# Optimization experiments

Hardware: AMD Instinct MI355X
Metric: run time of the kernel (lower is better)

The kernel has to match this reference:

```python
import jax, jax.numpy as jnp
import numpy as np

N, E = 50000, 800000
IN, HID, OUT, HEADS = 256, 128, 256, 4
CAT = HEADS * HID  # 512


def _gat(x, ei_src, ei_dst, W, a_src, a_dst, b, heads, out_ch, concat):
    """PyG-style GATConv with self-loops. x:[N,F]; returns [N,heads*out_ch] or [N,out_ch]."""
    n = x.shape[0]
    loop = jnp.arange(n, dtype=ei_src.dtype)
    src = jnp.concatenate([ei_src, loop])
    dst = jnp.concatenate([ei_dst, loop])
    h = (x @ W).reshape(n, heads, out_ch)              # [N,H,C]
    al_s = jnp.einsum('nhc,hc->nh', h, a_src)          # [N,H]
    al_d = jnp.einsum('nhc,hc->nh', h, a_dst)
    e = jax.nn.leaky_relu(al_s[src] + al_d[dst], 0.2)  # [E',H]
    emax = jax.ops.segment_max(e, dst, num_segments=n)
    ee = jnp.exp(e - emax[dst])
    denom = jax.ops.segment_sum(ee, dst, num_segments=n)
    alpha = ee / (denom[dst] + 1e-16)                  # segment softmax over incoming edges
    out = jax.ops.segment_sum(h[src] * alpha[:, :, None], dst, num_segments=n)  # [N,H,C]
    out = out.reshape(n, heads * out_ch) if concat else out.mean(axis=1)
    return out + b


def setup_inputs() -> dict:
    key = jax.random.key(0)
    ks = jax.random.split(key, 20)
    g = lambda k, shape, fan: (jax.random.normal(k, shape, jnp.float32) / np.sqrt(fan)).astype(jnp.float32)
    return {
        'x': jax.random.normal(ks[0], (N, IN), jnp.float32),
        'edge_index': jax.random.randint(ks[1], (2, E), 0, N, dtype=jnp.int32),
        # GAT layer 1: IN -> HID x 4 heads, concat
        'W1': g(ks[2], (IN, CAT), IN), 'a_src1': g(ks[3], (HEADS, HID), HID),
        'a_dst1': g(ks[4], (HEADS, HID), HID), 'b1': jnp.zeros((CAT,), jnp.float32),
        # GAT layer 2: CAT -> HID x 4 heads, concat
        'W2': g(ks[5], (CAT, CAT), CAT), 'a_src2': g(ks[6], (HEADS, HID), HID),
        'a_dst2': g(ks[7], (HEADS, HID), HID), 'b2': jnp.zeros((CAT,), jnp.float32),
        # GAT layer 3: CAT -> OUT, 1 head, no concat
        'W3': g(ks[8], (CAT, OUT), CAT), 'a_src3': g(ks[9], (1, OUT), OUT),
        'a_dst3': g(ks[10], (1, OUT), OUT), 'b3': jnp.zeros((OUT,), jnp.float32),
        # response_generator MLP: OUT -> 2*HID -> HID -> OUT
        'M1': g(ks[11], (OUT, 2 * HID), OUT), 'mb1': jnp.zeros((2 * HID,), jnp.float32),
        'M2': g(ks[12], (2 * HID, HID), 2 * HID), 'mb2': jnp.zeros((HID,), jnp.float32),
        'M3': g(ks[13], (HID, OUT), HID), 'mb3': jnp.zeros((OUT,), jnp.float32),
    }


def reference(x, edge_index, W1, a_src1, a_dst1, b1, W2, a_src2, a_dst2, b2,
              W3, a_src3, a_dst3, b3, M1, mb1, M2, mb2, M3, mb3):
    src, dst = edge_index[0], edge_index[1]
    h = _gat(x, src, dst, W1, a_src1, a_dst1, b1, HEADS, HID, True)
    h = jax.nn.elu(h)  # dropout is identity in eval mode
    h = _gat(h, src, dst, W2, a_src2, a_dst2, b2, HEADS, HID, True)
    h = jax.nn.elu(h)
    h = _gat(h, src, dst, W3, a_src3, a_dst3, b3, 1, OUT, False)
    # response generator MLP (dropout identity in eval)
    r = jax.nn.relu(h @ M1 + mb1)
    r = jax.nn.relu(r @ M2 + mb2)
    return r @ M3 + mb3
```

## Files before the change

### kernel.cpp

```cpp
#include <hip/hip_runtime.h>
#include <cstdint>
#include <cstddef>

#define HEADS  4
#define HIDC   128
#define CATF   512
#define IN_F   256
#define OUT_F  256

typedef _Float16 f16x8 __attribute__((ext_vector_type(8)));
typedef _Float16 f16x4 __attribute__((ext_vector_type(4)));
typedef float f32x4  __attribute__((ext_vector_type(4)));

__device__ __forceinline__ void async16(const void* g, void* l) {
    __builtin_amdgcn_global_load_lds((const __attribute__((address_space(1))) void*)g,
                                     (__attribute__((address_space(3))) void*)l, 16, 0, 0);
}

__global__ void init_counts(int* cnt, int N) {
    int i = blockIdx.x * blockDim.x + threadIdx.x;
    if (i < N) cnt[i] = 1;
}

__global__ void count_dst(const int* __restrict__ dst, int E, int* cnt) {
    int i = blockIdx.x * blockDim.x + threadIdx.x;
    if (i < E) atomicAdd(&cnt[dst[i]], 1);
}

__global__ void scan_partial(const int* __restrict__ cnt, int* excl, int* bsum, int N) {
    __shared__ int tmp[256];
    int i = blockIdx.x * 256 + threadIdx.x;
    int v = (i < N) ? cnt[i] : 0;
    tmp[threadIdx.x] = v;
    __syncthreads();
    for (int off = 1; off < 256; off <<= 1) {
        int t = ((int)threadIdx.x >= off) ? tmp[threadIdx.x - off] : 0;
        __syncthreads();
        tmp[threadIdx.x] += t;
        __syncthreads();
    }
    if (i < N) excl[i] = tmp[threadIdx.x] - v;
    if (threadIdx.x == 255) bsum[blockIdx.x] = tmp[255];
}

__global__ void scan_bsums(int* bsum, int nb) {
    __shared__ int tmp[256];
    int v = ((int)threadIdx.x < nb) ? bsum[threadIdx.x] : 0;
    tmp[threadIdx.x] = v;
    __syncthreads();
    for (int off = 1; off < 256; off <<= 1) {
        int t = ((int)threadIdx.x >= off) ? tmp[threadIdx.x - off] : 0;
        __syncthreads();
        tmp[threadIdx.x] += t;
        __syncthreads();
    }
    if ((int)threadIdx.x < nb) bsum[threadIdx.x] = tmp[threadIdx.x] - v;
}

__global__ void add_carry(int* indptr, int* pos, const int* __restrict__ bsum, int N, int total) {
    int i = blockIdx.x * blockDim.x + threadIdx.x;
    if (i < N) {
        int v = indptr[i] + bsum[i >> 8];
        indptr[i] = v;
        pos[i] = v;
    }
    if (i == 0) indptr[N] = total;
}

__global__ void scatter_edges(const int* __restrict__ src, const int* __restrict__ dst,
                              int E, int N, int* pos, int* esrc) {
    int i = blockIdx.x * blockDim.x + threadIdx.x;
    int total = E + N;
    if (i >= total) return;
    int s, d;
    if (i < E) { s = src[i]; d = dst[i]; }
    else       { s = i - E;  d = s; }
    int p = atomicAdd(&pos[d], 1);
    esrc[p] = s;
}

__global__ void conv_h16(const float* __restrict__ in, _Float16* __restrict__ out, long n4) {
    long i = (long)blockIdx.x * blockDim.x + threadIdx.x;
    if (i >= n4) return;
    float4 v = ((const float4*)in)[i];
    f16x4 o = { (_Float16)v.x, (_Float16)v.y, (_Float16)v.z, (_Float16)v.w };
    ((f16x4*)out)[i] = o;
}

struct WDesc { const float* W; _Float16* hi; _Float16* lo; int K; int N; int off; };
struct WPack { WDesc d[6]; int total; };
__global__ void conv_w_all(WPack p) {
    int idx = blockIdx.x * blockDim.x + threadIdx.x;
    if (idx >= p.total) return;
    int wi = 0;
    while (wi < 5 && idx >= p.d[wi + 1].off) wi++;
    const WDesc& w = p.d[wi];
    int li = idx - w.off;
    int n = li / w.K, k = li - n * w.K;
    float v = w.W[(size_t)k * w.N + n];
    _Float16 h = (_Float16)v;
    w.hi[(size_t)n * w.K + k] = h;
    if (w.lo) w.lo[(size_t)n * w.K + k] = (_Float16)(v - (float)h);
}

__global__ void zero2(float* a, float* b, int n) {
    int i = blockIdx.x * blockDim.x + threadIdx.x;
    if (i < n) { a[i] = 0.f; b[i] = 0.f; }
}

#define TM 128
#define TN 128
#define TK 32
template <int MODE, int NMF, int ATTN>
__global__ __launch_bounds__(256) void gemm_bt(
        const _Float16* __restrict__ A,
        const _Float16* __restrict__ Bh, const _Float16* __restrict__ Bl,
        const float* __restrict__ bias,
        float* __restrict__ out_f, _Float16* __restrict__ out_h16,
        const float* __restrict__ asrc, const float* __restrict__ adst,
        float* __restrict__ al_s, float* __restrict__ al_d,
        int M, int N, int K, int act) {
    __shared__ __align__(16) char smem[(NMF == 2 ? 49152 : 32768) + (ATTN ? 2048 : 16)];
    _Float16* sA  = (_Float16*)smem;
    _Float16* sBh = (_Float16*)(smem + 16384);
    _Float16* sBl = (_Float16*)(smem + 32768);
    float* sred   = (float*)(smem + (NMF == 2 ? 49152 : 32768));

    int tid = threadIdx.x;
    int wave = tid >> 6, lane = tid & 63;
    int nwg = gridDim.x * gridDim.y;
    int id  = blockIdx.y * gridDim.x + blockIdx.x;
    int qq = nwg >> 3, rr = nwg & 7;
    int xcd = id & 7, li = id >> 3;
    int wg = (xcd < rr ? xcd * (qq + 1) : rr * (qq + 1) + (xcd - rr) * qq) + li;
    int by = wg / (int)gridDim.x;
    int bx = wg - by * (int)gridDim.x;
    int m0 = by * TM, n0 = bx * TN;
    int wm = wave >> 1, wn = wave & 1;
    int srow = lane >> 2;
    int skel = (lane & 3) * 8;
    int fr = lane & 15, quad = lane >> 4;

    f32x4 acc[4][4];
#pragma unroll
    for (int i = 0; i < 4; i++)
#pragma unroll
        for (int j = 0; j < 4; j++) acc[i][j] = (f32x4){0.f, 0.f, 0.f, 0.f};

    auto stage = [&](int buf, int k0) {
#pragma unroll
        for (int c = 0; c < 2; c++) {
            int chunk = wave * 2 + c;
            int r = chunk * 16 + srow;
            int gmA = m0 + r; if (gmA >= M) gmA = M - 1;
            int gnB = n0 + r;
            size_t aoff = (size_t)gmA * K + k0 + skel;
            size_t boff = (size_t)gnB * K + k0 + skel;
            int ldso = buf * (TM * TK) + chunk * 512;
            async16(A + aoff, &sA[ldso]);
            async16(Bh + boff, &sBh[ldso]);
            if (NMF == 2) async16(Bl + boff, &sBl[ldso]);
        }
    };

    const int nsteps = K / TK;
    stage(0, 0);
    int cur = 0;
    for (int s = 0; s < nsteps; ++s, cur ^= 1) {
        if (s + 1 < nsteps) {
            stage(cur ^ 1, (s + 1) * TK);
            if (NMF == 2) asm volatile("s_waitcnt vmcnt(6)" ::: "memory");
            else          asm volatile("s_waitcnt vmcnt(4)" ::: "memory");
        } else {
            asm volatile("s_waitcnt vmcnt(0)" ::: "memory");
        }
        __builtin_amdgcn_s_barrier();
        __builtin_amdgcn_sched_barrier(0);

        f16x8 fa[4], fbh[4], fbl[4];
#pragma unroll
        for (int i = 0; i < 4; i++) {
            int ra = cur * (TM * TK) + (wm * 64 + i * 16 + fr) * TK + quad * 8;
            int rb = cur * (TN * TK) + (wn * 64 + i * 16 + fr) * TK + quad * 8;
            fa[i]  = *(const f16x8*)&sA[ra];
            fbh[i] = *(const f16x8*)&sBh[rb];
            if (NMF == 2) fbl[i] = *(const f16x8*)&sBl[rb];
        }
#pragma unroll
        for (int i = 0; i < 4; i++)
#pragma unroll
            for (int j = 0; j < 4; j++) {
                if (NMF == 2)
                    acc[i][j] = __builtin_amdgcn_mfma_f32_16x16x32_f16(fa[i], fbl[j], acc[i][j], 0, 0, 0);
                acc[i][j] = __builtin_amdgcn_mfma_f32_16x16x32_f16(fa[i], fbh[j], acc[i][j], 0, 0, 0);
            }
        __builtin_amdgcn_sched_barrier(0);
        __builtin_amdgcn_s_barrier();
    }

    float avs[4], avd[4], bv[4];
#pragma unroll
    for (int j = 0; j < 4; j++) {
        int gn = n0 + wn * 64 + j * 16 + fr;
        if (ATTN) { avs[j] = asrc[gn]; avd[j] = adst[gn]; }
        bv[j] = bias ? bias[gn] : 0.f;
    }

    if (ATTN) {
#pragma unroll
        for (int i = 0; i < 4; i++)
#pragma unroll
            for (int r = 0; r < 4; r++) {
                float ps = 0.f, pd = 0.f;
#pragma unroll
                for (int j = 0; j < 4; j++) {
                    float v = acc[i][j][r];
                    ps += v * avs[j]; pd += v * avd[j];
                }
#pragma unroll
                for (int off = 1; off < 16; off <<= 1) {
                    ps += __shfl_xor(ps, off);
                    pd += __shfl_xor(pd, off);
                }
                if (fr == 0) {
                    int lrow = wm * 64 + i * 16 + quad * 4 + r;
                    sred[lrow * 4 + 0 * 2 + wn] = ps;
                    sred[lrow * 4 + 1 * 2 + wn] = pd;
                }
            }
    }

    if (MODE == 1) {
#pragma unroll
        for (int i = 0; i < 4; i++)
#pragma unroll
            for (int r = 0; r < 4; r++) {
                int gm = m0 + wm * 64 + i * 16 + quad * 4 + r;
                if (gm >= M) continue;
#pragma unroll
                for (int j = 0; j < 4; j++) {
                    int gn = n0 + wn * 64 + j * 16 + fr;
                    float v = acc[i][j][r] + bv[j];
                    if (act == 1) v = fmaxf(v, 0.f);
                    out_f[(size_t)gm * N + gn] = v;
                }
            }
        __syncthreads();
    } else {
        _Float16* cst = (_Float16*)smem;
#pragma unroll
        for (int i = 0; i < 4; i++) {
            int svb = ((wm * 16 + i * 4 + quad) << 1) & 15;
#pragma unroll
            for (int j = 0; j < 4; j++) {
#pragma unroll
                for (int r = 0; r < 4; r++) {
                    int row = wm * 64 + i * 16 + quad * 4 + r;
                    int col = wn * 64 + j * 16 + fr;
                    float v = acc[i][j][r] + bv[j];
                    if (act == 1) v = fmaxf(v, 0.f);
                    int blk = (col >> 3) ^ svb;
                    cst[row * 128 + (blk << 3) + (col & 7)] = (_Float16)v;
                }
            }
        }
        __syncthreads();
#pragma unroll
        for (int q = 0; q < 8; q++) {
            int c = tid + 256 * q;
            int row = c >> 4, b = c & 15;
            int gm = m0 + row;
            if (gm < M) {
                int svb = ((row >> 2) << 1) & 15;
                f16x8 val = *(const f16x8*)&cst[row * 128 + ((b ^ svb) << 3)];
                *(f16x8*)&out_h16[(size_t)gm * N + n0 + b * 8] = val;
            }
        }
    }

    if (ATTN) {
        if (tid < TM) {
            int gm = m0 + tid;
            if (gm < M) {
                float s = sred[tid * 4 + 0] + sred[tid * 4 + 1];
                float d = sred[tid * 4 + 2] + sred[tid * 4 + 3];
                if (ATTN == 1) {
                    int head = n0 >> 7;
                    al_s[gm * HEADS + head] = s;
                    al_d[gm * HEADS + head] = d;
                } else {
                    atomicAdd(&al_s[gm], s);
                    atomicAdd(&al_d[gm], d);
                }
            }
        }
    }
}

template <int CT, int H>
__global__ void gat_aggregate_f(const _Float16* __restrict__ h,
                                const float* __restrict__ al_s, const float* __restrict__ al_d,
                                const int* __restrict__ indptr, const int* __restrict__ esrc,
                                const float* __restrict__ bias,
                                _Float16* __restrict__ oh,
                                int N, int act) {
    typedef _Float16 hvec __attribute__((ext_vector_type(CT)));
    const int C_ALL = CT * 64;
    int n = (blockIdx.x * blockDim.x + threadIdx.x) >> 6;
    int lane = threadIdx.x & 63;
    if (n >= N) return;
    int head = (lane * H) >> 6;
    float ald = al_d[n * H + head];
    float acc[CT];
#pragma unroll
    for (int k = 0; k < CT; k++) acc[k] = 0.f;
    float dsum = 0.f;

    int beg = indptr[n], end = indptr[n + 1];
    int idx = beg;
    for (; idx + 8 <= end; idx += 8) {
        int s[8]; float av[8]; hvec v[8];
#pragma unroll
        for (int u = 0; u < 8; u++) s[u] = esrc[idx + u];
#pragma unroll
        for (int u = 0; u < 8; u++) av[u] = al_s[s[u] * H + head];
#pragma unroll
        for (int u = 0; u < 8; u++) v[u] = *(const hvec*)(h + (size_t)s[u] * C_ALL + lane * CT);
#pragma unroll
        for (int u = 0; u < 8; u++) {
            float e = av[u] + ald;
            e = e > 0.f ? e : 0.2f * e;
            e = fminf(e, 60.f);
            float w = __expf(e);
            dsum += w;
#pragma unroll
            for (int k = 0; k < CT; k++) acc[k] += w * (float)v[u][k];
        }
    }
    if (idx + 4 <= end) {
        int s[4]; float av[4]; hvec v[4];
#pragma unroll
        for (int u = 0; u < 4; u++) s[u] = esrc[idx + u];
#pragma unroll
        for (int u = 0; u < 4; u++) av[u] = al_s[s[u] * H + head];
#pragma unroll
        for (int u = 0; u < 4; u++) v[u] = *(const hvec*)(h + (size_t)s[u] * C_ALL + lane * CT);
#pragma unroll
        for (int u = 0; u < 4; u++) {
            float e = av[u] + ald;
            e = e > 0.f ? e : 0.2f * e;
            e = fminf(e, 60.f);
            float w = __expf(e);
            dsum += w;
#pragma unroll
            for (int k = 0; k < CT; k++) acc[k] += w * (float)v[u][k];
        }
        idx += 4;
    }
    for (; idx < end; idx++) {
        int s0 = esrc[idx];
        float e = al_s[s0 * H + head] + ald;
        e = e > 0.f ? e : 0.2f * e;
        e = fminf(e, 60.f);
        float w = __expf(e);
        dsum += w;
        hvec v0 = *(const hvec*)(h + (size_t)s0 * C_ALL + lane * CT);
#pragma unroll
        for (int k = 0; k < CT; k++) acc[k] += w * (float)v0[k];
    }

    float inv = 1.f / (dsum + 1e-16f);
    size_t ob = (size_t)n * C_ALL + lane * CT;
    const float* bp = bias + lane * CT;
    hvec o;
#pragma unroll
    for (int k = 0; k < CT; k++) {
        float v = acc[k] * inv + bp[k];
        if (act == 1) v = v > 0.f ? v : (__expf(v) - 1.f);
        o[k] = (_Float16)v;
    }
    __builtin_nontemporal_store(o, (hvec*)(oh + ob));
}

extern "C" void kernel_launch(void* const* d_in, const int* in_sizes, int n_in,
                              void* d_out, int out_size, void* d_ws, size_t ws_size,
                              hipStream_t stream) {
    const float* x   = (const float*)d_in[0];
    const int*   ei  = (const int*)d_in[1];
    const float* W1  = (const float*)d_in[2];
    const float* as1 = (const float*)d_in[3];
    const float* ad1 = (const float*)d_in[4];
    const float* b1  = (const float*)d_in[5];
    const float* W2  = (const float*)d_in[6];
    const float* as2 = (const float*)d_in[7];
    const float* ad2 = (const float*)d_in[8];
    const float* b2  = (const float*)d_in[9];
    const float* W3  = (const float*)d_in[10];
    const float* as3 = (const float*)d_in[11];
    const float* ad3 = (const float*)d_in[12];
    const float* b3  = (const float*)d_in[13];
    const float* M1  = (const float*)d_in[14];
    const float* mb1 = (const float*)d_in[15];
    const float* M2  = (const float*)d_in[16];
    const float* mb2 = (const float*)d_in[17];
    const float* M3  = (const float*)d_in[18];
    const float* mb3 = (const float*)d_in[19];
    float* out = (float*)d_out;

    const int N = in_sizes[0] / IN_F;
    const int E = in_sizes[1] / 2;
    const int* src = ei;
    const int* dst = ei + E;

    char* ws = (char*)d_ws;
    auto alloc = [&](size_t bytes) { char* p = ws; ws += (bytes + 255) & ~(size_t)255; return p; };
    _Float16* H16 = (_Float16*)alloc((size_t)N * CATF * 2);
    _Float16* P16 = (_Float16*)alloc((size_t)N * CATF * 2);
    float* al_s = (float*)alloc((size_t)N * HEADS * 4);
    float* al_d = (float*)alloc((size_t)N * HEADS * 4);
    int* cnt    = (int*)alloc((size_t)N * 4);
    int* pos    = (int*)alloc((size_t)N * 4);
    int* indptr = (int*)alloc((size_t)(N + 1) * 4);
    int* esrc   = (int*)alloc((size_t)(E + N) * 4);
    int* bsum   = (int*)alloc(256 * 4);
    auto walloc = [&](int k, int n, _Float16*& h, _Float16*& l, bool need_lo) {
        h = (_Float16*)alloc((size_t)k * n * 2);
        l = need_lo ? (_Float16*)alloc((size_t)k * n * 2) : nullptr;
    };
    _Float16 *W1h, *W1l, *W2h, *W2l, *W3h, *W3l, *M1h, *M1l, *M2h, *M2l, *M3h, *M3l;
    walloc(IN_F, CATF, W1h, W1l, false);
    walloc(CATF, CATF, W2h, W2l, false);
    walloc(CATF, OUT_F, W3h, W3l, false);
    walloc(OUT_F, 2 * HIDC, M1h, M1l, true);
    walloc(2 * HIDC, HIDC, M2h, M2l, true);
    walloc(HIDC, OUT_F, M3h, M3l, true);

    const int nb = (N + 255) / 256;
    init_counts<<<(N + 255) / 256, 256, 0, stream>>>(cnt, N);
    count_dst<<<(E + 255) / 256, 256, 0, stream>>>(dst, E, cnt);
    scan_partial<<<nb, 256, 0, stream>>>(cnt, indptr, bsum, N);
    scan_bsums<<<1, 256, 0, stream>>>(bsum, nb);
    add_carry<<<nb, 256, 0, stream>>>(indptr, pos, bsum, N, E + N);
    scatter_edges<<<(E + N + 255) / 256, 256, 0, stream>>>(src, dst, E, N, pos, esrc);

    {
        WPack p;
        int off = 0;
        auto setd = [&](int i, const float* W, _Float16* h, _Float16* l, int K, int Nc) {
            p.d[i] = WDesc{W, h, l, K, Nc, off};
            off += K * Nc;
        };
        setd(0, W1, W1h, W1l, IN_F, CATF);
        setd(1, W2, W2h, W2l, CATF, CATF);
        setd(2, W3, W3h, W3l, CATF, OUT_F);
        setd(3, M1, M1h, M1l, OUT_F, 2 * HIDC);
        setd(4, M2, M2h, M2l, 2 * HIDC, HIDC);
        setd(5, M3, M3h, M3l, HIDC, OUT_F);
        p.total = off;
        conv_w_all<<<(off + 255) / 256, 256, 0, stream>>>(p);
    }

    auto gemm_gat = [&](const _Float16* Ap, const _Float16* Bhp, _Float16* oh,
                        const float* asrc, const float* adst, int M_, int Nc, int K, int attn_mode) {
        dim3 grid(Nc / TN, (M_ + TM - 1) / TM);
        if (attn_mode == 1)
            gemm_bt<2, 1, 1><<<grid, 256, 0, stream>>>(Ap, Bhp, nullptr, nullptr, nullptr, oh,
                                                       asrc, adst, al_s, al_d, M_, Nc, K, 0);
        else
            gemm_bt<2, 1, 2><<<grid, 256, 0, stream>>>(Ap, Bhp, nullptr, nullptr, nullptr, oh,
                                                       asrc, adst, al_s, al_d, M_, Nc, K, 0);
    };
    auto gemm_mlp16 = [&](const _Float16* Ap, const _Float16* Bhp, const _Float16* Blp,
                          const float* bias, _Float16* oh, int M_, int Nc, int K, int act) {
        dim3 grid(Nc / TN, (M_ + TM - 1) / TM);
        gemm_bt<2, 2, 0><<<grid, 256, 0, stream>>>(Ap, Bhp, Blp, bias, nullptr, oh,
                                                   nullptr, nullptr, nullptr, nullptr, M_, Nc, K, act);
    };

    const int gwav = (N + 3) / 4;

    conv_h16<<<((long)N * IN_F / 4 + 255) / 256, 256, 0, stream>>>(x, P16, (long)N * IN_F / 4);

    gemm_gat(P16, W1h, H16, as1, ad1, N, CATF, IN_F, 1);
    gat_aggregate_f<8, HEADS><<<gwav, 256, 0, stream>>>(H16, al_s, al_d, indptr, esrc,
                                                        b1, P16, N, 1);
    gemm_gat(P16, W2h, H16, as2, ad2, N, CATF, CATF, 1);
    gat_aggregate_f<8, HEADS><<<gwav, 256, 0, stream>>>(H16, al_s, al_d, indptr, esrc,
                                                        b2, P16, N, 1);
    zero2<<<(N + 255) / 256, 256, 0, stream>>>(al_s, al_d, N);
    gemm_gat(P16, W3h, H16, as3, ad3, N, OUT_F, CATF, 2);
    gat_aggregate_f<4, 1><<<gwav, 256, 0, stream>>>(H16, al_s, al_d, indptr, esrc,
                                                    b3, P16, N, 0);
    _Float16* Q16 = H16;
    _Float16* R16 = P16 + (size_t)N * OUT_F;
    gemm_mlp16(P16, M1h, M1l, mb1, Q16, N, 2 * HIDC, OUT_F, 1);
    gemm_mlp16(Q16, M2h, M2l, mb2, R16, N, HIDC, 2 * HIDC, 1);
    {
        dim3 grid(OUT_F / TN, (N + TM - 1) / TM);
        gemm_bt<1, 2, 0><<<grid, 256, 0, stream>>>(R16, M3h, M3l, mb3, out, nullptr,
                                                   nullptr, nullptr, nullptr, nullptr,
                                                   N, OUT_F, HIDC, 0);
    }
}
```

Measured before the change: 736.3 us.

## Triple-buffer GEMM K-loop for single-precision-B path and replace init kernels with memsets

For the NMF==1 GEMM path (the GAT projection GEMMs), the shared-memory staging moves from double to triple buffering, prefetching two K-steps ahead with adjusted vmcnt waits, so more global-load latency can be hidden. Shared memory for that path grows from 32KB to 48KB, which may reduce occupancy. Separately, the count init and the zeroing kernels become hipMemsetAsync calls, with the self-loop +1 folded into the scan, removing two small kernel launches.

Result: no change. 744.0 us (+1.0%).

```diff
diff --git a/kernel.cpp b/kernel.cpp
--- a/kernel.cpp
+++ b/kernel.cpp
@@ -17,11 +17,6 @@
                                      (__attribute__((address_space(3))) void*)l, 16, 0, 0);
 }
 
-__global__ void init_counts(int* cnt, int N) {
-    int i = blockIdx.x * blockDim.x + threadIdx.x;
-    if (i < N) cnt[i] = 1;
-}
-
 __global__ void count_dst(const int* __restrict__ dst, int E, int* cnt) {
     int i = blockIdx.x * blockDim.x + threadIdx.x;
     if (i < E) atomicAdd(&cnt[dst[i]], 1);
@@ -30,7 +25,7 @@
 __global__ void scan_partial(const int* __restrict__ cnt, int* excl, int* bsum, int N) {
     __shared__ int tmp[256];
     int i = blockIdx.x * 256 + threadIdx.x;
-    int v = (i < N) ? cnt[i] : 0;
+    int v = (i < N) ? cnt[i] + 1 : 0;
     tmp[threadIdx.x] = v;
     __syncthreads();
     for (int off = 1; off < 256; off <<= 1) {
@@ -103,11 +98,6 @@
     if (w.lo) w.lo[(size_t)n * w.K + k] = (_Float16)(v - (float)h);
 }
 
-__global__ void zero2(float* a, float* b, int n) {
-    int i = blockIdx.x * blockDim.x + threadIdx.x;
-    if (i < n) { a[i] = 0.f; b[i] = 0.f; }
-}
-
 #define TM 128
 #define TN 128
 #define TK 32
@@ -120,11 +110,12 @@
         const float* __restrict__ asrc, const float* __restrict__ adst,
         float* __restrict__ al_s, float* __restrict__ al_d,
         int M, int N, int K, int act) {
-    __shared__ __align__(16) char smem[(NMF == 2 ? 49152 : 32768) + (ATTN ? 2048 : 16)];
+    const int NBUF = (NMF == 1) ? 3 : 2;
+    __shared__ __align__(16) char smem[49152 + (ATTN ? 2048 : 16)];
     _Float16* sA  = (_Float16*)smem;
-    _Float16* sBh = (_Float16*)(smem + 16384);
+    _Float16* sBh = (_Float16*)(smem + (NMF == 1 ? 24576 : 16384));
     _Float16* sBl = (_Float16*)(smem + 32768);
-    float* sred   = (float*)(smem + (NMF == 2 ? 49152 : 32768));
+    float* sred   = (float*)(smem + 49152);
 
     int tid = threadIdx.x;
     int wave = tid >> 6, lane = tid & 63;
@@ -164,19 +155,22 @@
     };
 
     const int nsteps = K / TK;
+    const int L = (NMF == 2) ? 6 : 4;
     stage(0, 0);
-    int cur = 0;
-    for (int s = 0; s < nsteps; ++s, cur ^= 1) {
-        if (s + 1 < nsteps) {
-            stage(cur ^ 1, (s + 1) * TK);
-            if (NMF == 2) asm volatile("s_waitcnt vmcnt(6)" ::: "memory");
-            else          asm volatile("s_waitcnt vmcnt(4)" ::: "memory");
-        } else {
-            asm volatile("s_waitcnt vmcnt(0)" ::: "memory");
-        }
+    if (NBUF == 3) stage(1, TK);
+    for (int s = 0; s < nsteps; ++s) {
+        int pf = s + NBUF - 1;
+        if (pf < nsteps) stage(pf % NBUF, pf * TK);
+        int fut = nsteps - 1 - s; if (fut > NBUF - 1) fut = NBUF - 1;
+        int cnt = fut * L;
+        if (cnt >= 8)      asm volatile("s_waitcnt vmcnt(8)" ::: "memory");
+        else if (cnt == 6) asm volatile("s_waitcnt vmcnt(6)" ::: "memory");
+        else if (cnt == 4) asm volatile("s_waitcnt vmcnt(4)" ::: "memory");
+        else               asm volatile("s_waitcnt vmcnt(0)" ::: "memory");
         __builtin_amdgcn_s_barrier();
         __builtin_amdgcn_sched_barrier(0);
 
+        int cur = (NBUF == 3) ? (s % 3) : (s & 1);
         f16x8 fa[4], fbh[4], fbl[4];
 #pragma unroll
         for (int i = 0; i < 4; i++) {
@@ -436,7 +430,7 @@
     walloc(HIDC, OUT_F, M3h, M3l, true);
 
     const int nb = (N + 255) / 256;
-    init_counts<<<(N + 255) / 256, 256, 0, stream>>>(cnt, N);
+    hipMemsetAsync(cnt, 0, (size_t)N * 4, stream);
     count_dst<<<(E + 255) / 256, 256, 0, stream>>>(dst, E, cnt);
     scan_partial<<<nb, 256, 0, stream>>>(cnt, indptr, bsum, N);
     scan_bsums<<<1, 256, 0, stream>>>(bsum, nb);
@@ -487,7 +481,8 @@
     gemm_gat(P16, W2h, H16, as2, ad2, N, CATF, CATF, 1);
     gat_aggregate_f<8, HEADS><<<gwav, 256, 0, stream>>>(H16, al_s, al_d, indptr, esrc,
                                                         b2, P16, N, 1);
-    zero2<<<(N + 255) / 256, 256, 0, stream>>>(al_s, al_d, N);
+    hipMemsetAsync(al_s, 0, (size_t)N * 4, stream);
+    hipMemsetAsync(al_d, 0, (size_t)N * 4, stream);
     gemm_gat(P16, W3h, H16, as3, ad3, N, OUT_F, CATF, 2);
     gat_aggregate_f<4, 1><<<gwav, 256, 0, stream>>>(H16, al_s, al_d, indptr, esrc,
                                                     b3, P16, N, 0);
```
